# Performance work log

Hardware: AMD Instinct MI355X
Metric: run time of the kernel (lower is better)

The kernel has to match this reference:

```python
import jax, jax.numpy as jnp
import numpy as np

H, HD, D = 16, 64, 1024
SCALE = HD ** -0.5
TEMP = 1.0
EPS = 1e-5

def setup_inputs() -> dict:
    key = jax.random.key(0)
    ks = jax.random.split(key, 10)
    B, N = 2, 2048
    lim = 1.0 / np.sqrt(D)
    def lin(k, out_d, in_d):
        k1, k2 = jax.random.split(k)
        W = jax.random.uniform(k1, (out_d, in_d), jnp.float32, -lim, lim)
        b = jax.random.uniform(k2, (out_d,), jnp.float32, -lim, lim)
        return W, b
    Wq, bq = lin(ks[0], H * HD, D)
    Wk, bk = lin(ks[1], H * HD, D)
    Wv, bv = lin(ks[2], H * HD, D)
    Wo, bo = lin(ks[3], D, H * HD)
    return {
        "x": jax.random.normal(ks[4], (B, N, D), jnp.float32),
        "adaptive_scale": jnp.ones((H,), jnp.float32),
        "Wq": Wq, "bq": bq, "Wk": Wk, "bk": bk, "Wv": Wv, "bv": bv,
        "Wo": Wo, "bo": bo,
        "gamma": jnp.ones((D,), jnp.float32),
        "beta": jnp.zeros((D,), jnp.float32),
    }

def reference(x, adaptive_scale, Wq, bq, Wk, bk, Wv, bv, Wo, bo, gamma, beta):
    B, N, _ = x.shape
    # self-attention: context = x
    Q = (x @ Wq.T + bq).reshape(B, N, H, HD)
    K = (x @ Wk.T + bk).reshape(B, N, H, HD)
    V = (x @ Wv.T + bv).reshape(B, N, H, HD)
    # per-head adaptive scale folded into scores (matches naive QK^T * scale / temp)
    scores = jnp.einsum('bnhd,bmhd->bhnm', Q, K)
    scores = scores * (SCALE * adaptive_scale)[None, :, None, None] / TEMP
    w = jax.nn.softmax(scores, axis=-1)  # [B,H,N,N]
    attn = jnp.einsum('bhnm,bmhd->bnhd', w, V).reshape(B, N, H * HD)
    y = x + (attn @ Wo.T + bo)
    mu = jnp.mean(y, axis=-1, keepdims=True)
    var = jnp.var(y, axis=-1, keepdims=True)
    return (y - mu) / jnp.sqrt(var + EPS) * gamma + beta
```

## Files before the change

kernel.cpp:

```cpp
#include <hip/hip_runtime.h>
#include <hip/hip_bf16.h>

using bf16 = __hip_bfloat16;
typedef __attribute__((ext_vector_type(8))) short short8;
typedef __attribute__((ext_vector_type(4))) short short4v;
typedef __attribute__((ext_vector_type(4))) float f32x4;

#define MFMA16(a, b, c) __builtin_amdgcn_mfma_f32_16x16x32_bf16((a), (b), (c), 0, 0, 0)

__device__ inline void async16(bf16* lds, const bf16* g) {
  __builtin_amdgcn_global_load_lds(
      (const __attribute__((address_space(1))) void*)g,
      (__attribute__((address_space(3))) void*)lds, 16, 0, 0);
}

__device__ inline short bfs(float x) {
  union { bf16 h; short s; } u; u.h = __float2bfloat16(x); return u.s;
}
__device__ inline short4v pack4(float a, float b, float c, float d) {
  short4v r; r[0] = bfs(a); r[1] = bfs(b); r[2] = bfs(c); r[3] = bfs(d); return r;
}
__device__ inline unsigned pkt2(float x, float y) {
  return __builtin_amdgcn_perm(__float_as_uint(y), __float_as_uint(x), 0x07060302u);
}
__device__ inline float ex2(float x) {
  float r; asm("v_exp_f32 %0, %1" : "=v"(r) : "v"(x)); return r;
}
__device__ inline void pl32swap(unsigned& a, unsigned& b) {
  asm("v_permlane32_swap_b32 %0, %1" : "+v"(a), "+v"(b));
}
__device__ inline void pl16swap(unsigned& a, unsigned& b) {
  asm("v_permlane16_swap_b32 %0, %1" : "+v"(a), "+v"(b));
}

__global__ __launch_bounds__(256) void cvt_all(
    const float* __restrict__ x,  const float* __restrict__ Wq,
    const float* __restrict__ Wk, const float* __restrict__ Wv,
    const float* __restrict__ Wo,
    bf16* __restrict__ xb, bf16* __restrict__ Wqb, bf16* __restrict__ Wkb,
    bf16* __restrict__ Wvb, bf16* __restrict__ Wob) {
  int i = blockIdx.x * 256 + threadIdx.x;
  const float* s; bf16* d; int off;
  if (i < 1048576)      { s = x;  d = xb;  off = i; }
  else if (i < 1310720) { s = Wq; d = Wqb; off = i - 1048576; }
  else if (i < 1572864) { s = Wk; d = Wkb; off = i - 1310720; }
  else if (i < 1835008) { s = Wv; d = Wvb; off = i - 1572864; }
  else                  { s = Wo; d = Wob; off = i - 1835008; }
  float4 v = ((const float4*)s)[off];
  short4v o = pack4(v.x, v.y, v.z, v.w);
  *(short4v*)&d[(size_t)off * 4] = o;
}

__global__ __launch_bounds__(256) void gemm_qkv(
    const bf16* __restrict__ A,
    const bf16* __restrict__ Wq, const bf16* __restrict__ Wk, const bf16* __restrict__ Wv,
    const float* __restrict__ bq, const float* __restrict__ bk, const float* __restrict__ bv,
    const float* __restrict__ asc,
    bf16* __restrict__ Qb, bf16* __restrict__ Kb, bf16* __restrict__ Vtb) {
  __shared__ __align__(16) bf16 As[128 * 64];
  __shared__ __align__(16) bf16 Bs[128 * 64];
  __shared__ __align__(16) bf16 scrT[4][16 * 72];

  const int tid = threadIdx.x;
  const int lane = tid & 63;
  const int w = tid >> 6;
  const int m0 = blockIdx.x * 128;
  const int region = blockIdx.y >> 3;
  const int n0loc = (blockIdx.y & 7) * 128;
  const int wm = (w >> 1) * 64;
  const int wn = (w & 1) * 64;
  const int rq = lane & 15;
  const int quad = lane >> 4;

  const bf16* W = region == 0 ? Wq : (region == 1 ? Wk : Wv);
  const float* bias = region == 0 ? bq : (region == 1 ? bk : bv);
  bf16* C = region == 0 ? Qb : (region == 1 ? Kb : Vtb);

  f32x4 acc[4][4] = {};
  const bf16* Ag = A + (size_t)m0 * 1024;
  const bf16* Wg = W + (size_t)n0loc * 1024;

  const int srow = lane >> 3;
  const int sws = ((lane & 7) ^ srow) * 8;
  const int c0 = (quad ^ (rq & 7)) * 8;

  for (int k0 = 0; k0 < 1024; k0 += 64) {
    __syncthreads();
#pragma unroll
    for (int t = 0; t < 4; ++t) {
      int rb = w * 32 + t * 8;
      int row = rb + srow;
      async16(&As[rb * 64 + lane * 8], Ag + (size_t)row * 1024 + k0 + sws);
      async16(&Bs[rb * 64 + lane * 8], Wg + (size_t)row * 1024 + k0 + sws);
    }
    __syncthreads();

#pragma unroll
    for (int ks = 0; ks < 2; ++ks) {
      int off = c0 ^ (ks * 32);
      short8 a[4], b[4];
#pragma unroll
      for (int i = 0; i < 4; ++i) a[i] = *(const short8*)&As[(wm + i * 16 + rq) * 64 + off];
#pragma unroll
      for (int j = 0; j < 4; ++j) b[j] = *(const short8*)&Bs[(wn + j * 16 + rq) * 64 + off];
#pragma unroll
      for (int i = 0; i < 4; ++i)
#pragma unroll
        for (int j = 0; j < 4; ++j) acc[i][j] = MFMA16(a[i], b[j], acc[i][j]);
    }
  }

  const float LOG2E = 1.44269504088896f;
  if (region < 2) {
#pragma unroll
    for (int i = 0; i < 4; ++i)
#pragma unroll
      for (int j = 0; j < 4; ++j)
#pragma unroll
        for (int r2 = 0; r2 < 4; ++r2) {
          int m = m0 + wm + i * 16 + quad * 4 + r2;
          int nr = n0loc + wn + j * 16 + rq;
          int bb = m >> 11, t = m & 2047, h = nr >> 6, hd = nr & 63;
          float v = acc[i][j][r2] + bias[nr];
          if (region == 0) v *= 0.125f * asc[h] * LOG2E;
          C[(((size_t)(bb * 16 + h)) * 2048 + t) * 64 + hd] = __float2bfloat16(v);
        }
  } else {
    const int bb = m0 >> 11;
    const int h = (n0loc + wn) >> 6;
    const int tbase = (m0 & 2047) + wm;
    bf16* scr = scrT[w];
#pragma unroll
    for (int j = 0; j < 4; ++j) {
      int nr = n0loc + wn + j * 16 + rq;
      float bi = bias[nr];
#pragma unroll
      for (int i = 0; i < 4; ++i) {
        short4v pv = pack4(acc[i][j][0] + bi, acc[i][j][1] + bi,
                           acc[i][j][2] + bi, acc[i][j][3] + bi);
        *(short4v*)&scr[rq * 72 + i * 16 + quad * 4] = pv;
      }
#pragma unroll
      for (int pp = 0; pp < 4; ++pp) {
        int hdl = pp * 4 + quad;
        short4v v4 = *(const short4v*)&scr[hdl * 72 + rq * 4];
        size_t addr = (((size_t)(bb * 16 + h)) * 64 + j * 16 + hdl) * 2048 + tbase + rq * 4;
        *(short4v*)&C[addr] = v4;
      }
    }
  }
}

__global__ __launch_bounds__(256) void gemm_out(
    const bf16* __restrict__ A, const bf16* __restrict__ W,
    const float* __restrict__ bias, const float* __restrict__ R,
    float* __restrict__ Y) {
  __shared__ __align__(16) bf16 As[64 * 64];
  __shared__ __align__(16) bf16 Bs[128 * 64];

  const int tid = threadIdx.x;
  const int lane = tid & 63;
  const int w = tid >> 6;
  const int m0 = blockIdx.x * 64;
  const int n0 = blockIdx.y * 128;
  const int wm = (w >> 1) * 32;
  const int wn = (w & 1) * 64;
  const int rq = lane & 15;
  const int quad = lane >> 4;

  f32x4 acc[2][4] = {};
  const bf16* Ag = A + (size_t)m0 * 1024;
  const bf16* Wg = W + (size_t)n0 * 1024;

  const int srow = lane >> 3;
  const int sws = ((lane & 7) ^ srow) * 8;
  const int c0 = (quad ^ (rq & 7)) * 8;

  for (int k0 = 0; k0 < 1024; k0 += 64) {
    __syncthreads();
#pragma unroll
    for (int t = 0; t < 2; ++t) {
      int rb = w * 16 + t * 8;
      int row = rb + srow;
      async16(&As[rb * 64 + lane * 8], Ag + (size_t)row * 1024 + k0 + sws);
    }
#pragma unroll
    for (int t = 0; t < 4; ++t) {
      int rb = w * 32 + t * 8;
      int row = rb + srow;
      async16(&Bs[rb * 64 + lane * 8], Wg + (size_t)row * 1024 + k0 + sws);
    }
    __syncthreads();

#pragma unroll
    for (int ks = 0; ks < 2; ++ks) {
      int off = c0 ^ (ks * 32);
      short8 a[2], b[4];
#pragma unroll
      for (int i = 0; i < 2; ++i) a[i] = *(const short8*)&As[(wm + i * 16 + rq) * 64 + off];
#pragma unroll
      for (int j = 0; j < 4; ++j) b[j] = *(const short8*)&Bs[(wn + j * 16 + rq) * 64 + off];
#pragma unroll
      for (int i = 0; i < 2; ++i)
#pragma unroll
        for (int j = 0; j < 4; ++j) acc[i][j] = MFMA16(a[i], b[j], acc[i][j]);
    }
  }

#pragma unroll
  for (int i = 0; i < 2; ++i)
#pragma unroll
    for (int j = 0; j < 4; ++j)
#pragma unroll
      for (int r2 = 0; r2 < 4; ++r2) {
        int m = m0 + wm + i * 16 + quad * 4 + r2;
        int n = n0 + wn + j * 16 + rq;
        Y[(size_t)m * 1024 + n] = acc[i][j][r2] + bias[n] + R[(size_t)m * 1024 + n];
      }
}

__global__ __launch_bounds__(256, 4) void attn_kernel(
    const bf16* __restrict__ Qb, const bf16* __restrict__ Kb,
    const bf16* __restrict__ Vtb,
    bf16* __restrict__ P0, bf16* __restrict__ P1, float* __restrict__ lbuf) {
  __shared__ __align__(16) bf16 Ks[64 * 64];
  __shared__ __align__(16) bf16 Vs[64 * 64];

  const int wid = blockIdx.x + (blockIdx.y << 4) + (blockIdx.z << 8);
  const int sid = (wid & 7) * 128 + (wid >> 3);
  const int q0 = (sid & 15) * 128;
  const int h = (sid >> 4) & 15;
  const int zz = sid >> 8;
  const int b = zz & 1;
  const int half = zz >> 1;

  const int tid = threadIdx.x;
  const int lane = tid & 63;
  const int w = tid >> 6;
  const int rq = lane & 15;
  const int quad = lane >> 4;

  const size_t head = ((size_t)(b * 16 + h)) * 2048 * 64;
  const bf16* Qh = Qb + head;
  const bf16* Kh = Kb + head;
  const bf16* Vh = Vtb + head;

  short8 aq[2][2];
#pragma unroll
  for (int s = 0; s < 2; ++s) {
    const bf16* qrow = Qh + (size_t)(q0 + w * 32 + s * 16 + rq) * 64;
    aq[s][0] = *(const short8*)&qrow[quad * 8];
    aq[s][1] = *(const short8*)&qrow[quad * 8 + 32];
  }

  short8 ones;
#pragma unroll
  for (int i = 0; i < 8; ++i) ones[i] = (short)0x3F80;

  const int srow = lane >> 3;
  const int swsV = ((lane & 7) ^ srow) * 8;
  const int c0 = (quad ^ (rq & 7)) * 8;
  const int c1 = c0 ^ 32;
  const int kc0 = (quad ^ (rq >> 1)) * 8;
  const int kc1 = kc0 ^ 32;

  f32x4 accO[2][4] = {};
  f32x4 lacc[2] = {};

  const int kt0 = half * 16;
  for (int kt = kt0; kt < kt0 + 16; ++kt) {
    __syncthreads();
#pragma unroll
    for (int t = 0; t < 2; ++t) {
      int rb = w * 16 + t * 8;
      int row = rb + srow;
      int swsK = ((lane & 7) ^ ((row >> 1) & 7)) * 8;
      async16(&Ks[rb * 64 + lane * 8], Kh + (size_t)(kt * 64 + row) * 64 + swsK);
      async16(&Vs[rb * 64 + lane * 8], Vh + (size_t)row * 2048 + kt * 64 + swsV);
    }
    __syncthreads();

    f32x4 S[2][4] = {};
    __builtin_amdgcn_s_setprio(1);
#pragma unroll
    for (int c = 0; c < 4; ++c) {
      const bf16* kr = &Ks[(c * 16 + rq) * 64];
      short8 k0 = *(const short8*)&kr[kc0];
      short8 k1 = *(const short8*)&kr[kc1];
      S[0][c] = MFMA16(k0, aq[0][0], S[0][c]);
      S[0][c] = MFMA16(k1, aq[0][1], S[0][c]);
      S[1][c] = MFMA16(k0, aq[1][0], S[1][c]);
      S[1][c] = MFMA16(k1, aq[1][1], S[1][c]);
    }
    __builtin_amdgcn_s_setprio(0);

    unsigned W[2][8];
#pragma unroll
    for (int s = 0; s < 2; ++s)
#pragma unroll
      for (int c = 0; c < 4; ++c) {
        W[s][c * 2 + 0] = pkt2(ex2(S[s][c][0]), ex2(S[s][c][1]));
        W[s][c * 2 + 1] = pkt2(ex2(S[s][c][2]), ex2(S[s][c][3]));
      }

    short8 ap[2][2];
#pragma unroll
    for (int s = 0; s < 2; ++s) {
      pl32swap(W[s][0], W[s][2]); pl32swap(W[s][1], W[s][3]);
      pl32swap(W[s][4], W[s][6]); pl32swap(W[s][5], W[s][7]);
      pl16swap(W[s][0], W[s][2]); pl16swap(W[s][1], W[s][3]);
      pl16swap(W[s][4], W[s][6]); pl16swap(W[s][5], W[s][7]);
      union { unsigned u[4]; short8 v; } f0, f1;
      f0.u[0] = W[s][0]; f0.u[1] = W[s][1]; f0.u[2] = W[s][2]; f0.u[3] = W[s][3];
      f1.u[0] = W[s][4]; f1.u[1] = W[s][5]; f1.u[2] = W[s][6]; f1.u[3] = W[s][7];
      ap[s][0] = f0.v; ap[s][1] = f1.v;
    }

    __builtin_amdgcn_s_setprio(1);
#pragma unroll
    for (int dt = 0; dt < 4; ++dt) {
      const bf16* vr = &Vs[(dt * 16 + rq) * 64];
      short8 v0 = *(const short8*)&vr[c0];
      short8 v1 = *(const short8*)&vr[c1];
      accO[0][dt] = MFMA16(ap[0][0], v0, accO[0][dt]);
      accO[0][dt] = MFMA16(ap[0][1], v1, accO[0][dt]);
      accO[1][dt] = MFMA16(ap[1][0], v0, accO[1][dt]);
      accO[1][dt] = MFMA16(ap[1][1], v1, accO[1][dt]);
    }
#pragma unroll
    for (int s = 0; s < 2; ++s) {
      lacc[s] = MFMA16(ap[s][0], ones, lacc[s]);
      lacc[s] = MFMA16(ap[s][1], ones, lacc[s]);
    }
    __builtin_amdgcn_s_setprio(0);
  }

  bf16* Pout = half ? P1 : P0;
  float* lout = lbuf + half * 65536;
#pragma unroll
  for (int s = 0; s < 2; ++s) {
#pragma unroll
    for (int dt = 0; dt < 4; ++dt)
#pragma unroll
      for (int r = 0; r < 4; ++r) {
        int t = q0 + w * 32 + s * 16 + quad * 4 + r;
        int d = dt * 16 + rq;
        Pout[((size_t)(b * 2048 + t)) * 1024 + h * 64 + d] =
            __float2bfloat16(accO[s][dt][r]);
      }
    if (rq == 0) {
#pragma unroll
      for (int r = 0; r < 4; ++r) {
        int t = q0 + w * 32 + s * 16 + quad * 4 + r;
        lout[(b * 16 + h) * 2048 + t] = lacc[s][r];
      }
    }
  }
}

__global__ __launch_bounds__(256) void combine_kernel(
    bf16* __restrict__ P0, const bf16* __restrict__ P1,
    const float* __restrict__ lbuf) {
  const int row = blockIdx.x;
  const int tid = threadIdx.x;
  const int col = tid * 4;
  const int b = row >> 11, t = row & 2047;
  const int h = col >> 6;
  const float l = lbuf[(b * 16 + h) * 2048 + t] + lbuf[65536 + (b * 16 + h) * 2048 + t];
  const float rl = 1.f / l;
  size_t base = (size_t)row * 1024 + col;
  short4v p0 = *(const short4v*)&P0[base];
  short4v p1 = *(const short4v*)&P1[base];
  union { short s; bf16 h; } u;
  float v[4];
#pragma unroll
  for (int i = 0; i < 4; ++i) {
    u.s = p0[i]; float a = __bfloat162float(u.h);
    u.s = p1[i]; float c = __bfloat162float(u.h);
    v[i] = (a + c) * rl;
  }
  *(short4v*)&P0[base] = pack4(v[0], v[1], v[2], v[3]);
}

__global__ __launch_bounds__(256) void ln_kernel(
    const float* __restrict__ Y, const float* __restrict__ gamma,
    const float* __restrict__ beta, float* __restrict__ out) {
  const int row = blockIdx.x;
  const int tid = threadIdx.x;
  const int lane = tid & 63;
  const int w = tid >> 6;
  const float* y = Y + (size_t)row * 1024;

  float4 v = *(const float4*)&y[tid * 4];
  float s = v.x + v.y + v.z + v.w;
  float ss = v.x * v.x + v.y * v.y + v.z * v.z + v.w * v.w;
#pragma unroll
  for (int msk = 1; msk < 64; msk <<= 1) {
    s += __shfl_xor(s, msk);
    ss += __shfl_xor(ss, msk);
  }
  __shared__ float red[2][4];
  if (lane == 0) { red[0][w] = s; red[1][w] = ss; }
  __syncthreads();
  s = red[0][0] + red[0][1] + red[0][2] + red[0][3];
  ss = red[1][0] + red[1][1] + red[1][2] + red[1][3];
  float mean = s * (1.f / 1024.f);
  float var = ss * (1.f / 1024.f) - mean * mean;
  float rstd = rsqrtf(var + 1e-5f);
  float4 g = *(const float4*)&gamma[tid * 4];
  float4 bt = *(const float4*)&beta[tid * 4];
  float4 o;
  o.x = (v.x - mean) * rstd * g.x + bt.x;
  o.y = (v.y - mean) * rstd * g.y + bt.y;
  o.z = (v.z - mean) * rstd * g.z + bt.z;
  o.w = (v.w - mean) * rstd * g.w + bt.w;
  *(float4*)&out[(size_t)row * 1024 + tid * 4] = o;
}

extern "C" void kernel_launch(void* const* d_in, const int* in_sizes, int n_in,
                              void* d_out, int out_size, void* d_ws, size_t ws_size,
                              hipStream_t stream) {
  const float* x     = (const float*)d_in[0];
  const float* asc   = (const float*)d_in[1];
  const float* Wq    = (const float*)d_in[2];
  const float* bq    = (const float*)d_in[3];
  const float* Wk    = (const float*)d_in[4];
  const float* bk    = (const float*)d_in[5];
  const float* Wv    = (const float*)d_in[6];
  const float* bv    = (const float*)d_in[7];
  const float* Wo    = (const float*)d_in[8];
  const float* bo    = (const float*)d_in[9];
  const float* gamma = (const float*)d_in[10];
  const float* beta  = (const float*)d_in[11];
  float* out = (float*)d_out;

  char* ws = (char*)d_ws;
  const size_t MB = 1024 * 1024;
  bf16* Qb   = (bf16*)(ws);
  bf16* Kb   = (bf16*)(ws + 8 * MB);
  bf16* Vtb  = (bf16*)(ws + 16 * MB);
  bf16* attn = (bf16*)(ws + 24 * MB);
  bf16* xb   = (bf16*)(ws + 32 * MB);
  bf16* Wqb  = (bf16*)(ws + 40 * MB);
  bf16* Wkb  = (bf16*)(ws + 42 * MB);
  bf16* Wvb  = (bf16*)(ws + 44 * MB);
  bf16* Wob  = (bf16*)(ws + 46 * MB);
  float* y   = (float*)(ws);
  bf16* P1   = xb;
  float* lbuf = (float*)Wqb;

  cvt_all<<<dim3(8192), dim3(256), 0, stream>>>(x, Wq, Wk, Wv, Wo, xb, Wqb, Wkb, Wvb, Wob);
  gemm_qkv<<<dim3(32, 24), dim3(256), 0, stream>>>(xb, Wqb, Wkb, Wvb, bq, bk, bv, asc, Qb, Kb, Vtb);
  attn_kernel<<<dim3(16, 16, 4), dim3(256), 0, stream>>>(Qb, Kb, Vtb, attn, P1, lbuf);
  combine_kernel<<<dim3(4096), dim3(256), 0, stream>>>(attn, P1, lbuf);
  gemm_out<<<dim3(64, 8), dim3(256), 0, stream>>>(attn, Wob, bo, x, y);
  ln_kernel<<<dim3(4096), dim3(256), 0, stream>>>(y, gamma, beta, out);
}
```

Baseline: 206.5 us.

## Fuse split-KV attention combine into output projection GEMM A-tile load

Removes the separate combine kernel and instead has gemm_out load both partial attention outputs and the softmax denominators, sum and normalize them in registers, and write the result swizzled into LDS as the A tile. The A loads for the next k-step are prefetched into registers during the current step. This drops one launch plus a full read-modify-write pass over the attention buffer. In exchange each GEMM block reads twice the A data and recomputes the normalization once per column tile (8x redundancy), and the A path moves from async global-to-LDS copies to a register staging path.

```diff
diff --git a/kernel.cpp b/kernel.cpp
--- a/kernel.cpp
+++ b/kernel.cpp
@@ -25,6 +25,9 @@
 }
 __device__ inline float ex2(float x) {
   float r; asm("v_exp_f32 %0, %1" : "=v"(r) : "v"(x)); return r;
+}
+__device__ inline float frcp(float x) {
+  float r; asm("v_rcp_f32 %0, %1" : "=v"(r) : "v"(x)); return r;
 }
 __device__ inline void pl32swap(unsigned& a, unsigned& b) {
   asm("v_permlane32_swap_b32 %0, %1" : "+v"(a), "+v"(b));
@@ -152,7 +155,8 @@
 }
 
 __global__ __launch_bounds__(256) void gemm_out(
-    const bf16* __restrict__ A, const bf16* __restrict__ W,
+    const bf16* __restrict__ P0, const bf16* __restrict__ P1,
+    const float* __restrict__ lbuf, const bf16* __restrict__ W,
     const float* __restrict__ bias, const float* __restrict__ R,
     float* __restrict__ Y) {
   __shared__ __align__(16) bf16 As[64 * 64];
@@ -169,27 +173,61 @@
   const int quad = lane >> 4;
 
   f32x4 acc[2][4] = {};
-  const bf16* Ag = A + (size_t)m0 * 1024;
   const bf16* Wg = W + (size_t)n0 * 1024;
 
   const int srow = lane >> 3;
-  const int sws = ((lane & 7) ^ srow) * 8;
+  const int lc = lane & 7;
+  const int sws = (lc ^ srow) * 8;
   const int c0 = (quad ^ (rq & 7)) * 8;
-
+  const int bb = m0 >> 11;
+
+  short8 rp0[2], rp1[2];
+  float rl[2];
+
+  auto loadA = [&](int k0) {
+    int h = k0 >> 6;
+#pragma unroll
+    for (int t = 0; t < 2; ++t) {
+      int row = w * 16 + t * 8 + srow;
+      int m = m0 + row;
+      size_t src = (size_t)m * 1024 + k0 + lc * 8;
+      rp0[t] = *(const short8*)&P0[src];
+      rp1[t] = *(const short8*)&P1[src];
+      int tkn = m & 2047;
+      float l0 = lbuf[(bb * 16 + h) * 2048 + tkn];
+      float l1 = lbuf[65536 + (bb * 16 + h) * 2048 + tkn];
+      rl[t] = frcp(l0 + l1);
+    }
+  };
+
+  loadA(0);
   for (int k0 = 0; k0 < 1024; k0 += 64) {
     __syncthreads();
-#pragma unroll
-    for (int t = 0; t < 2; ++t) {
-      int rb = w * 16 + t * 8;
-      int row = rb + srow;
-      async16(&As[rb * 64 + lane * 8], Ag + (size_t)row * 1024 + k0 + sws);
-    }
 #pragma unroll
     for (int t = 0; t < 4; ++t) {
       int rb = w * 32 + t * 8;
       int row = rb + srow;
       async16(&Bs[rb * 64 + lane * 8], Wg + (size_t)row * 1024 + k0 + sws);
     }
+#pragma unroll
+    for (int t = 0; t < 2; ++t) {
+      int row = w * 16 + t * 8 + srow;
+      union { short8 v; unsigned u[4]; } a, b;
+      a.v = rp0[t]; b.v = rp1[t];
+      unsigned out[4];
+#pragma unroll
+      for (int j = 0; j < 4; ++j) {
+        float alo = __uint_as_float(a.u[j] << 16);
+        float ahi = __uint_as_float(a.u[j] & 0xffff0000u);
+        float blo = __uint_as_float(b.u[j] << 16);
+        float bhi = __uint_as_float(b.u[j] & 0xffff0000u);
+        out[j] = pkt2((alo + blo) * rl[t], (ahi + bhi) * rl[t]);
+      }
+      union { unsigned u[4]; short8 v; } o;
+      o.u[0] = out[0]; o.u[1] = out[1]; o.u[2] = out[2]; o.u[3] = out[3];
+      *(short8*)&As[row * 64 + (lc ^ srow) * 8] = o.v;
+    }
+    if (k0 + 64 < 1024) loadA(k0 + 64);
     __syncthreads();
 
 #pragma unroll
@@ -356,30 +394,6 @@
       }
     }
   }
-}
-
-__global__ __launch_bounds__(256) void combine_kernel(
-    bf16* __restrict__ P0, const bf16* __restrict__ P1,
-    const float* __restrict__ lbuf) {
-  const int row = blockIdx.x;
-  const int tid = threadIdx.x;
-  const int col = tid * 4;
-  const int b = row >> 11, t = row & 2047;
-  const int h = col >> 6;
-  const float l = lbuf[(b * 16 + h) * 2048 + t] + lbuf[65536 + (b * 16 + h) * 2048 + t];
-  const float rl = 1.f / l;
-  size_t base = (size_t)row * 1024 + col;
-  short4v p0 = *(const short4v*)&P0[base];
-  short4v p1 = *(const short4v*)&P1[base];
-  union { short s; bf16 h; } u;
-  float v[4];
-#pragma unroll
-  for (int i = 0; i < 4; ++i) {
-    u.s = p0[i]; float a = __bfloat162float(u.h);
-    u.s = p1[i]; float c = __bfloat162float(u.h);
-    v[i] = (a + c) * rl;
-  }
-  *(short4v*)&P0[base] = pack4(v[0], v[1], v[2], v[3]);
 }
 
 __global__ __launch_bounds__(256) void ln_kernel(
@@ -452,7 +466,6 @@
   cvt_all<<<dim3(8192), dim3(256), 0, stream>>>(x, Wq, Wk, Wv, Wo, xb, Wqb, Wkb, Wvb, Wob);
   gemm_qkv<<<dim3(32, 24), dim3(256), 0, stream>>>(xb, Wqb, Wkb, Wvb, bq, bk, bv, asc, Qb, Kb, Vtb);
   attn_kernel<<<dim3(16, 16, 4), dim3(256), 0, stream>>>(Qb, Kb, Vtb, attn, P1, lbuf);
-  combine_kernel<<<dim3(4096), dim3(256), 0, stream>>>(attn, P1, lbuf);
-  gemm_out<<<dim3(64, 8), dim3(256), 0, stream>>>(attn, Wob, bo, x, y);
+  gemm_out<<<dim3(64, 8), dim3(256), 0, stream>>>(attn, P1, lbuf, Wob, bo, x, y);
   ln_kernel<<<dim3(4096), dim3(256), 0, stream>>>(y, gamma, beta, out);
 }
```

Measured after the change: 211.8 us. 1.03x slower.
